# Performance work log

Hardware: AMD Instinct MI355X
Metric: run time of the kernel (lower is better)

Reference implementation:

```python
import jax, jax.numpy as jnp
import numpy as np

B, N, K = 2, 2048, 30          # batch, residues, neighbors
DN, DE, L = 256, 128, 3        # dim_nodes, dim_edges, num_layers
NF, EF = 12, 28                # raw node / edge feature dims
EPS = 1e-6


def _gather(h, idx):
    # h: [B,N,D], idx: [B,N,K] -> [B,N,K,D]
    b, n, k = idx.shape
    d = h.shape[-1]
    return jnp.take_along_axis(h, idx.reshape(b, n * k, 1), axis=1).reshape(b, n, k, d)


def _nrm(v):
    return v / (jnp.linalg.norm(v, axis=-1, keepdims=True) + EPS)


def _forward(X, C, Wn, bn, We, be, Wm1, bm1, Wm2, bm2, Wue1, bue1, Wue2, bue2):
    mask_i = (C > 0).astype(X.dtype)                      # [B,N]
    Nat, CA, Cat, Oat = X[..., 0, :], X[..., 1, :], X[..., 2, :], X[..., 3, :]

    # local residue frames via Gram-Schmidt on (N, CA, C)
    u = _nrm(Cat - CA)
    v0 = Nat - CA
    v = _nrm(v0 - jnp.sum(v0 * u, -1, keepdims=True) * u)
    w = jnp.cross(u, v)
    R = jnp.stack([u, v, w], axis=-1)                     # [B,N,3,3]

    # node features: internal coords (unit bond vectors + log lengths)
    def bond_feat(bv):
        return jnp.concatenate([_nrm(bv), jnp.log(jnp.linalg.norm(bv, axis=-1, keepdims=True) + EPS)], -1)
    node_feat = jnp.concatenate([bond_feat(CA - Nat), bond_feat(Cat - CA), bond_feat(Oat - Cat)], -1)  # [B,N,12]
    node_h = (node_feat @ Wn + bn) * mask_i[..., None]

    # kNN graph on centroid distances (graph_distance_atom_type=-1)
    Xc = X.mean(axis=2)                                   # [B,N,3]
    D2 = jnp.sum((Xc[:, :, None] - Xc[:, None, :]) ** 2, -1)  # [B,N,N]
    BIG = 1e9
    D2 = D2 + BIG * (1.0 - mask_i)[:, None, :] + BIG * jnp.eye(N, dtype=X.dtype)[None]
    _, edge_idx = jax.lax.top_k(-D2, K)                   # [B,N,K]

    mask_j = _gather(mask_i[..., None], edge_idx)[..., 0]
    mask_ij = mask_i[..., None] * mask_j                  # [B,N,K]

    # edge features: RBF distances + local-frame direction + relative rotation
    xj = _gather(Xc, edge_idx)
    d = xj - Xc[:, :, None]                               # [B,N,K,3]
    dist = jnp.linalg.norm(d, axis=-1)
    local = jnp.einsum('bndc,bnkd->bnkc', R, d)           # R_i^T d
    dirv = local / (dist[..., None] + EPS)
    Rj = _gather(R.reshape(B, N, 9), edge_idx).reshape(B, N, K, 3, 3)
    Rrel = jnp.einsum('bnde,bnkdf->bnkef', R, Rj).reshape(B, N, K, 9)  # R_i^T R_j
    centers = jnp.linspace(0.0, 20.0, 16)
    sigma = 20.0 / 16.0
    rbf = jnp.exp(-(((dist[..., None] - centers) / sigma) ** 2))       # [B,N,K,16]
    edge_h = (jnp.concatenate([rbf, dirv, Rrel], -1) @ We + be) * mask_ij[..., None]

    # GNN message passing: gather -> MLP -> masked mean scatter, + edge update
    denom = jnp.sum(mask_ij, -1, keepdims=True) + EPS     # [B,N,1]
    for l in range(L):
        hj = _gather(node_h, edge_idx)                    # [B,N,K,DN]
        hi = jnp.broadcast_to(node_h[:, :, None], hj.shape)
        mi = jnp.concatenate([hi, hj, edge_h], -1)        # [B,N,K,2*DN+DE]
        m = jax.nn.softplus(mi @ Wm1[l] + bm1[l]) @ Wm2[l] + bm2[l]
        m = m * mask_ij[..., None]
        node_h = (node_h + m.sum(axis=2) / denom) * mask_i[..., None]
        e = jax.nn.softplus(mi @ Wue1[l] + bue1[l]) @ Wue2[l] + bue2[l]
        edge_h = (edge_h + e) * mask_ij[..., None]

    return node_h, edge_h, edge_idx, mask_i, mask_ij


def setup_inputs() -> dict:
    key = jax.random.key(0)
    ks = jax.random.split(key, 10)
    s = lambda i, shp: jax.random.normal(ks[i], shp, jnp.float32) * 0.05
    M = 2 * DN + DE
    inp = {
        'X': jax.random.normal(ks[0], (B, N, 4, 3), jnp.float32),
        'C': jax.random.randint(ks[1], (B, N), 0, 4),
        'Wn': s(2, (NF, DN)), 'bn': jnp.zeros((DN,), jnp.float32),
        'We': s(3, (EF, DE)), 'be': jnp.zeros((DE,), jnp.float32),
        'Wm1': s(4, (L, M, DN)), 'bm1': jnp.zeros((L, DN), jnp.float32),
        'Wm2': s(5, (L, DN, DN)), 'bm2': jnp.zeros((L, DN), jnp.float32),
        'Wue1': s(6, (L, M, DE)), 'bue1': jnp.zeros((L, DE), jnp.float32),
        'Wue2': s(7, (L, DE, DE)), 'bue2': jnp.zeros((L, DE), jnp.float32),
    }
    return inp


def reference(X, C, Wn, bn, We, be, Wm1, bm1, Wm2, bm2, Wue1, bue1, Wue2, bue2):
    return _forward(X, C, Wn, bn, We, be, Wm1, bm1, Wm2, bm2, Wue1, bue1, Wue2, bue2)
```

## Files before the change

### kernel.cpp

```cpp
#include <hip/hip_runtime.h>
#include <math.h>

#define Bdim 2
#define Nn   2048
#define Kn   30
#define KP   32
#define DNc  256
#define DEc  128
#define NODES (Bdim*Nn)
#define EDGES (Bdim*Nn*Kn)
#define RPAD  (NODES*KP)
#define EPSF 1e-6f

#define BK 64
#define LDA (BK+8)
#define LDA0 40
#define LDP 136

typedef __attribute__((ext_vector_type(8))) short short8;
typedef __attribute__((ext_vector_type(4))) short sh4;
typedef __attribute__((ext_vector_type(4))) float floatx4;

__device__ __forceinline__ float softplusf(float x){
    float e = __expf(-fabsf(x));
// ... 240 lines not shown
    const unsigned short* __restrict__ featp, const unsigned short* __restrict__ Wp,
    const float* __restrict__ be, const float* __restrict__ mask_pad,
    unsigned short* __restrict__ edge_pad)
{
    __shared__ __align__(16) unsigned short smem[128*LDP];
    __shared__ float smask[128];
    unsigned short* Als  = smem;
    unsigned short* Bls  = smem + 128*LDA0;
    unsigned short* tile = smem;

    int tid = threadIdx.x;
    int lane = tid & 63, wave = tid >> 6;
    int wm = wave >> 1, wn = wave & 1;

    {
        const unsigned short* Ab = featp + (size_t)blockIdx.x*128*32;
        #pragma unroll
        for (int it=0; it<2; ++it){
            int idx = it*256 + tid;
            int row = idx >> 2, q = idx & 3;
            *(float4*)(&Als[row*LDA0 + q*8]) = *(const float4*)(Ab + row*32 + q*8);
        }
        if (tid < 128){
            int row = tid;
            *(float4*)(&Bls[row*LDA0 + 0])  = *(const float4*)(Wp + row*32 + 0);
            *(float4*)(&Bls[row*LDA0 + 8])  = *(const float4*)(Wp + row*32 + 8);
            *(float4*)(&Bls[row*LDA0 + 16]) = *(const float4*)(Wp + row*32 + 16);
            *(float4*)(&Bls[row*LDA0 + 24]) = *(const float4*)(Wp + row*32 + 24);
        } else {
            smask[tid-128] = mask_pad[blockIdx.x*128 + (tid-128)];
        }
    }
    __syncthreads();

    floatx4 acc[4][4];
    #pragma unroll
    for (int i=0;i<4;++i)
        #pragma unroll
        for (int j=0;j<4;++j) acc[i][j] = (floatx4){0.f,0.f,0.f,0.f};
    short8 af[4], bf[4];
    int kidx = (lane>>4)*8;
    #pragma unroll
    for (int t=0;t<4;++t){
        int row = wm*64 + t*16 + (lane&15);
        af[t] = *(const short8*)(&Als[row*LDA0 + kidx]);
        int col = wn*64 + t*16 + (lane&15);
        bf[t] = *(const short8*)(&Bls[col*LDA0 + kidx]);
    }
    __syncthreads();
    #pragma unroll
    for (int i=0;i<4;++i)
        #pragma unroll
        for (int j=0;j<4;++j)
            acc[i][j] = __builtin_amdgcn_mfma_f32_16x16x32_bf16(bf[j], af[i], acc[i][j], 0,0,0);

    int quad = lane >> 4, cl = lane & 15;
    #pragma unroll
    for (int i=0;i<4;++i){
        int rowl = wm*64 + i*16 + cl;
        float mk = smask[rowl];
        #pragma unroll
        for (int j=0;j<4;++j){
            int coll = wn*64 + j*16 + quad*4;
            float4 bv = *(const float4*)&be[coll];
            sh4 w;
            w[0] = (short)f2bf((acc[i][j][0] + bv.x)*mk);
            w[1] = (short)f2bf((acc[i][j][1] + bv.y)*mk);
            w[2] = (short)f2bf((acc[i][j][2] + bv.z)*mk);
            w[3] = (short)f2bf((acc[i][j][3] + bv.w)*mk);
            *(sh4*)(&tile[rowl*LDP + coll]) = w;
        }
    }
    __syncthreads();
    {
        int rl = tid >> 1;
        int h  = tid & 1;
        unsigned short* dst = edge_pad + (size_t)(blockIdx.x*128 + rl)*128 + h*64;
        #pragma unroll
        for (int q=0; q<8; ++q)
            *(short8*)(dst + q*8) = *(const short8*)(&tile[rl*LDP + h*64 + q*8]);
    }
}

__global__ __launch_bounds__(256) void k_pack_we0(
    const float* __restrict__ We, unsigned short* __restrict__ Wp)
{
    int id = blockIdx.x*256 + threadIdx.x;
    if (id >= 128*32) return;
    int n = id >> 5, kk = id & 31;
    Wp[id] = (kk < 28) ? f2bf(We[kk*128 + n]) : 0;
}

__global__ __launch_bounds__(256) void k_pack_pqw(
    const float* __restrict__ Wm1, const float* __restrict__ Wue1,
    unsigned short* __restrict__ wPQw)
{
    int id = blockIdx.x*256 + threadIdx.x;
    if (id >= 3*768*256) return;
    int l = id / (768*256);
    int rem = id % (768*256);
    int n = rem >> 8, k = rem & 255;
    int c = (n < 384) ? n : n - 384;
    int r = (n < 384) ? k : 256 + k;
    float v = (c < 256) ? Wm1[((size_t)l*640 + r)*256 + c]
                        : Wue1[((size_t)l*640 + r)*128 + (c-256)];
    wPQw[id] = f2bf(v);
}

__global__ __launch_bounds__(256) void k_pack_ew(
    const float* __restrict__ Wm1, const float* __restrict__ Wue1,
    unsigned short* __restrict__ wEw)
{
    int id = blockIdx.x*256 + threadIdx.x;
    if (id >= 3*384*128) return;
    int l = id / (384*128);
    int rem = id % (384*128);
    int n = rem >> 7, k = rem & 127;
    int r = 512 + k;
    float v = (n < 256) ? Wm1[((size_t)l*640 + r)*256 + n]
                        : Wue1[((size_t)l*640 + r)*128 + (n-256)];
    wEw[id] = f2bf(v);
}

__global__ __launch_bounds__(256) void k_pack_ue2(
    const float* __restrict__ Wue2, unsigned short* __restrict__ wUe2w)
{
    int id = blockIdx.x*256 + threadIdx.x;
    if (id >= 3*128*128) return;
    int l = id / (128*128);
    int rem = id % (128*128);
    int n = rem >> 7, k = rem & 127;
    wUe2w[id] = f2bf(Wue2[((size_t)l*128 + k)*128 + n]);
}

__global__ __launch_bounds__(256) void k_pack_m2(
    const float* __restrict__ Wm2, unsigned short* __restrict__ wM2w)
{
    int id = blockIdx.x*256 + threadIdx.x;
    if (id >= 3*256*256) return;
    int l = id / (256*256);
    int rem = id % (256*256);
    int n = rem >> 8, k = rem & 255;
    wM2w[id] = f2bf(Wm2[((size_t)l*256 + k)*256 + n]);
}

template<int NR>
__device__ __forceinline__ void stage_tile_t(
    const unsigned short* __restrict__ gbase, int ldg, int k0,
    unsigned short* lds, int tid)
{
    #pragma unroll
    for (int it=0; it<NR/32; ++it){
        int idx = it*256 + tid;
        int row = idx >> 3;
        int ke  = (idx & 7) * 8;
        const float4* src = (const float4*)(gbase + (size_t)row*ldg + k0 + ke);
        *(float4*)(&lds[row*LDA + ke]) = *src;
    }
}

template<int TI, int TJ>
__device__ __forceinline__ void mma_tile_t(
    const unsigned short* Als, const unsigned short* Bls,
    int wm, int wn, int lane, floatx4 acc[TI][TJ])
{
    #pragma unroll
    for (int s=0; s<2; ++s){
        short8 af[TI], bf[TJ];
        int kidx = s*32 + (lane>>4)*8;
        #pragma unroll
        for (int t=0;t<TI;++t){
            int row = wm*(TI*16) + t*16 + (lane&15);
            af[t] = *(const short8*)(&Als[row*LDA + kidx]);
        }
        #pragma unroll
        for (int t=0;t<TJ;++t){
            int col = wn*(TJ*16) + t*16 + (lane&15);
            bf[t] = *(const short8*)(&Bls[col*LDA + kidx]);
        }
        #pragma unroll
        for (int i=0;i<TI;++i)
            #pragma unroll
            for (int j=0;j<TJ;++j)
                acc[i][j] = __builtin_amdgcn_mfma_f32_16x16x32_bf16(af[i], bf[j], acc[i][j], 0,0,0);
    }
}

template<int TI, int TJ>
__device__ __forceinline__ void mma_tile_sw(
    const unsigned short* Als, const unsigned short* Bls,
    int wm, int wn, int lane, floatx4 acc[TI][TJ])
{
    #pragma unroll
    for (int s=0; s<2; ++s){
        short8 af[TI], bf[TJ];
        int kidx = s*32 + (lane>>4)*8;
        #pragma unroll
        for (int t=0;t<TI;++t){
            int row = wm*(TI*16) + t*16 + (lane&15);
            af[t] = *(const short8*)(&Als[row*LDA + kidx]);
        }
        #pragma unroll
        for (int t=0;t<TJ;++t){
            int col = wn*(TJ*16) + t*16 + (lane&15);
            bf[t] = *(const short8*)(&Bls[col*LDA + kidx]);
        }
        #pragma unroll
        for (int i=0;i<TI;++i)
            #pragma unroll
            for (int j=0;j<TJ;++j)
                acc[i][j] = __builtin_amdgcn_mfma_f32_16x16x32_bf16(bf[j], af[i], acc[i][j], 0,0,0);
    }
}

__device__ __forceinline__ void mma_tileA_lp_sw(
    const unsigned short* Atile, const unsigned short* Bls,
    int k0, int wm, int wn, int lane, floatx4 acc[4][4])
{
    #pragma unroll
    for (int s=0; s<2; ++s){
        short8 af[4], bf[4];
        int kloc = s*32 + (lane>>4)*8;
        #pragma unroll
        for (int t=0;t<4;++t){
            int row = wm*64 + t*16 + (lane&15);
            af[t] = *(const short8*)(&Atile[row*LDP + k0 + kloc]);
            int col = wn*64 + t*16 + (lane&15);
            bf[t] = *(const short8*)(&Bls[col*LDA + kloc]);
        }
        #pragma unroll
        for (int i=0;i<4;++i)
            #pragma unroll
            for (int j=0;j<4;++j)
                acc[i][j] = __builtin_amdgcn_mfma_f32_16x16x32_bf16(bf[j], af[i], acc[i][j], 0,0,0);
    }
}

__global__ __launch_bounds__(256) void k_pq(
    const unsigned short* __restrict__ A, const unsigned short* __restrict__ Bw,
    unsigned short* __restrict__ PQbf,
    const float* __restrict__ bm1l, const float* __restrict__ bue1l)
{
    __shared__ __align__(16) unsigned short smem[(64+128)*LDA];
    unsigned short* Als = smem;
    unsigned short* Bls = smem + 64*LDA;
    unsigned short* tile = smem;
    int tid = threadIdx.x;
    int lane = tid & 63, wave = tid >> 6;
    int wm = wave >> 1, wn = wave & 1;
    const unsigned short* Ab = A + (size_t)blockIdx.x*64*256;
    const unsigned short* Bb = Bw + (size_t)blockIdx.y*128*256;
    floatx4 acc[2][4];
    #pragma unroll
    for (int i=0;i<2;++i)
        #pragma unroll
        for (int j=0;j<4;++j) acc[i][j] = (floatx4){0.f,0.f,0.f,0.f};
    for (int k0=0; k0<256; k0+=BK){
        stage_tile_t<64>(Ab, 256, k0, Als, tid);
        stage_tile_t<128>(Bb, 256, k0, Bls, tid);
        __syncthreads();
        mma_tile_sw<2,4>(Als, Bls, wm, wn, lane, acc);
        __syncthreads();
    }
    int quad = lane >> 4, cl = lane & 15;
    #pragma unroll
    for (int i=0;i<2;++i){
        int rowl = wm*32 + i*16 + cl;
        #pragma unroll
        for (int j=0;j<4;++j){
            int coll = wn*64 + j*16 + quad*4;
            int col0 = blockIdx.y*128 + coll;
            float4 bv;
            if (col0 < 256)      bv = *(const float4*)&bm1l[col0];
            else if (col0 < 384) bv = *(const float4*)&bue1l[col0-256];
            else                 bv = (float4){0.f,0.f,0.f,0.f};
            sh4 w;
            w[0] = (short)f2bf(acc[i][j][0] + bv.x);
            w[1] = (short)f2bf(acc[i][j][1] + bv.y);
            w[2] = (short)f2bf(acc[i][j][2] + bv.z);
            w[3] = (short)f2bf(acc[i][j][3] + bv.w);
            *(sh4*)(&tile[rowl*LDP + coll]) = w;
        }
    }
    __syncthreads();
    {
        int rl = tid >> 2;
        int h  = tid & 3;
        unsigned short* dst = PQbf + (size_t)(blockIdx.x*64 + rl)*768 + blockIdx.y*128 + h*32;
        #pragma unroll
        for (int q=0; q<4; ++q)
            *(short8*)(dst + q*8) = *(const short8*)(&tile[rl*LDP + h*32 + q*8]);
    }
}

__global__ __launch_bounds__(256) void k_h1s(
    const unsigned short* __restrict__ Apad, const unsigned short* __restrict__ Bw,
    const unsigned short* __restrict__ PQbf, const int* __restrict__ jg_pad,
    const float* __restrict__ mask_pad,
    unsigned short* __restrict__ Sout)
{
    __shared__ __align__(16) unsigned short smem[2*128*LDA];
    __shared__ float smask[128];
    unsigned short* Als = smem;
    unsigned short* Bls = smem + 128*LDA;
    unsigned short* pqT = smem;

    int tid = threadIdx.x;
    int lane = tid & 63, wave = tid >> 6;
    int wm = wave >> 1, wn = wave & 1;
    int colblk = blockIdx.y;

    const unsigned short* Ab = Apad + (size_t)blockIdx.x*128*128;
    const unsigned short* Bb = Bw + (size_t)colblk*128*128;
    floatx4 acc[4][4];
    #pragma unroll
    for (int i=0;i<4;++i)
        #pragma unroll
        for (int j=0;j<4;++j) acc[i][j] = (floatx4){0.f,0.f,0.f,0.f};
    for (int k0=0; k0<128; k0+=BK){
        stage_tile_t<128>(Ab, 128, k0, Als, tid);
        stage_tile_t<128>(Bb, 128, k0, Bls, tid);
        __syncthreads();
        mma_tile_t<4,4>(Als, Bls, wm, wn, lane, acc);
        __syncthreads();
    }

    {
        int colbase = colblk*128;
        #pragma unroll
        for (int it=0; it<2; ++it){
            int w    = it*256 + tid;
            int rq   = w & 31;
            int c8   = w >> 5;
            int row0 = rq*4;
            int r0   = blockIdx.x*128 + row0;
            int ni   = r0 >> 5;
            int4 jg4 = *(const int4*)&jg_pad[r0];
            int colg = colbase + c8*8;
            short8 pv = *(const short8*)(PQbf + (size_t)ni*768 + colg);
            short8 q0 = *(const short8*)(PQbf + (size_t)jg4.x*768 + 384 + colg);
            short8 q1 = *(const short8*)(PQbf + (size_t)jg4.y*768 + 384 + colg);
            short8 q2 = *(const short8*)(PQbf + (size_t)jg4.z*768 + 384 + colg);
            short8 q3 = *(const short8*)(PQbf + (size_t)jg4.w*768 + 384 + colg);
            #pragma unroll
            for (int q=0; q<8; ++q){
                float pf = bf2f((unsigned short)pv[q]);
                sh4 ov;
                ov[0] = (short)f2bf(pf + bf2f((unsigned short)q0[q]));
                ov[1] = (short)f2bf(pf + bf2f((unsigned short)q1[q]));
                ov[2] = (short)f2bf(pf + bf2f((unsigned short)q2[q]));
                ov[3] = (short)f2bf(pf + bf2f((unsigned short)q3[q]));
                *(sh4*)(&pqT[(c8*8 + q)*LDP + row0]) = ov;
            }
        }
        if (tid < 128) smask[tid] = mask_pad[blockIdx.x*128 + tid];
    }
    __syncthreads();

    int quad = lane >> 4, cl = lane & 15;
    float sumA[4] = {0.f,0.f,0.f,0.f};
    float sumB[4] = {0.f,0.f,0.f,0.f};
    #pragma unroll
    for (int i=0;i<4;++i){
        int rowl0 = wm*64 + i*16 + quad*4;
        float4 mk = *(const float4*)&smask[rowl0];
        float mkv[4] = {mk.x, mk.y, mk.z, mk.w};
        #pragma unroll
        for (int j=0;j<4;++j){
            int coll = wn*64 + j*16 + cl;
            sh4 pq4 = *(const sh4*)(&pqT[coll*LDP + rowl0]);
            #pragma unroll
            for (int rg=0; rg<4; ++rg){
                float v  = softplusf(acc[i][j][rg] + bf2f((unsigned short)pq4[rg]));
                float mv = mkv[rg]*v;
                if (i < 2) sumA[j] += mv; else sumB[j] += mv;
            }
        }
    }

    int nodeA = blockIdx.x*4 + wm*2;
    #pragma unroll
    for (int j=0;j<4;++j){
        float a = sumA[j];
        a += __shfl_xor(a, 16, 64);
        a += __shfl_xor(a, 32, 64);
        float b = sumB[j];
        b += __shfl_xor(b, 16, 64);
        b += __shfl_xor(b, 32, 64);
        int col = colblk*128 + wn*64 + j*16 + cl;
        if (quad == 0)      Sout[(size_t)nodeA*256 + col]     = f2bf(a);
        else if (quad == 1) Sout[(size_t)(nodeA+1)*256 + col] = f2bf(b);
    }
}

__global__ __launch_bounds__(256) void k_h1e(
    const unsigned short* __restrict__ Apad, const unsigned short* __restrict__ BwE,
    const unsigned short* __restrict__ BwU2,
    const unsigned short* __restrict__ PQbf, const int* __restrict__ jg_pad,
    const float* __restrict__ mask_pad, const float* __restrict__ bue2l,
    unsigned short* __restrict__ edge_pad, float* __restrict__ edge_f32,
    int last)
{
    __shared__ __align__(16) unsigned short smem[26624];
    unsigned short* Als  = smem;
    unsigned short* Bls  = smem + 128*LDA;
    unsigned short* tile = smem;
    unsigned short* B2   = smem + 128*LDP;

    int tid = threadIdx.x;
    int lane = tid & 63, wave = tid >> 6;
    int wm = wave >> 1, wn = wave & 1;

    const unsigned short* Ab = Apad + (size_t)blockIdx.x*128*128;
    floatx4 acc[4][4];
    #pragma unroll
    for (int i=0;i<4;++i)
        #pragma unroll
        for (int j=0;j<4;++j) acc[i][j] = (floatx4){0.f,0.f,0.f,0.f};
    for (int k0=0; k0<128; k0+=BK){
        stage_tile_t<128>(Ab, 128, k0, Als, tid);
        stage_tile_t<128>(BwE, 128, k0, Bls, tid);
        __syncthreads();
        mma_tile_sw<4,4>(Als, Bls, wm, wn, lane, acc);
        __syncthreads();
    }

    stage_tile_t<128>(BwU2, 128, 0, B2, tid);

    {
        int rl = tid >> 1;
        int h  = tid & 1;
        int r  = blockIdx.x*128 + rl;
        int ni = r >> 5;
        int jg = jg_pad[r];
        int cb = 256 + h*64;
        const unsigned short* Pr = PQbf + (size_t)ni*768 + cb;
        const unsigned short* Qr = PQbf + (size_t)jg*768 + 384 + cb;
        #pragma unroll
        for (int q=0; q<8; ++q){
            short8 pv = *(const short8*)(Pr + q*8);
            short8 qv = *(const short8*)(Qr + q*8);
            short8 ov;
            #pragma unroll
            for (int z=0; z<8; ++z)
                ov[z] = (short)f2bf(bf2f((unsigned short)pv[z]) + bf2f((unsigned short)qv[z]));
            *(short8*)(&tile[rl*LDP + h*64 + q*8]) = ov;
        }
    }
    __syncthreads();

    int quad = lane >> 4, cl = lane & 15;
    #pragma unroll
    for (int i=0;i<4;++i){
        int rowl = wm*64 + i*16 + cl;
        #pragma unroll
        for (int j=0;j<4;++j){
            int coll = wn*64 + j*16 + quad*4;
            sh4 pq4 = *(const sh4*)(&tile[rowl*LDP + coll]);
            sh4 hv;
            #pragma unroll
            for (int rg=0; rg<4; ++rg)
                hv[rg] = (short)f2bf(softplusf(acc[i][j][rg] + bf2f((unsigned short)pq4[rg])));
            *(sh4*)(&tile[rowl*LDP + coll]) = hv;
        }
    }
    __syncthreads();

    floatx4 acc2[4][4];
    #pragma unroll
    for (int i=0;i<4;++i)
        #pragma unroll
        for (int j=0;j<4;++j) acc2[i][j] = (floatx4){0.f,0.f,0.f,0.f};
    mma_tileA_lp_sw(tile, B2, 0, wm, wn, lane, acc2);
    __syncthreads();
    stage_tile_t<128>(BwU2, 128, 64, B2, tid);
    __syncthreads();
    mma_tileA_lp_sw(tile, B2, 64, wm, wn, lane, acc2);
    __syncthreads();

    float* sbias = (float*)B2;
    #pragma unroll
    for (int i=0;i<4;++i){
        int rowl = wm*64 + i*16 + cl;
        #pragma unroll
        for (int j=0;j<4;++j){
            int coll = wn*64 + j*16 + quad*4;
            sh4 w;
            #pragma unroll
            for (int rg=0; rg<4; ++rg) w[rg] = (short)f2bf(acc2[i][j][rg]);
            *(sh4*)(&tile[rowl*LDP + coll]) = w;
        }
    }
    if (tid < 128) sbias[tid] = bue2l[tid];
    __syncthreads();

    if (last){
        int c16  = lane & 31;
        int rsub = lane >> 5;
        #pragma unroll
        for (int step=0; step<16; ++step){
            int rowl = wave*32 + step*2 + rsub;
            int R = blockIdx.x*128 + rowl;
            int k = R & (KP-1);
            if (k < Kn){
                float mij = mask_pad[R];
                int node = R >> 5;
                int e = node*Kn + k;
                sh4 ov = *(const sh4*)(edge_pad + (size_t)R*128 + c16*4);
                sh4 av = *(const sh4*)(&tile[rowl*LDP + c16*4]);
                float4 bv = *(const float4*)(&sbias[c16*4]);
                float4 f;
                f.x = (bf2f((unsigned short)ov[0]) + bf2f((unsigned short)av[0]) + bv.x)*mij;
                f.y = (bf2f((unsigned short)ov[1]) + bf2f((unsigned short)av[1]) + bv.y)*mij;
                f.z = (bf2f((unsigned short)ov[2]) + bf2f((unsigned short)av[2]) + bv.z)*mij;
                f.w = (bf2f((unsigned short)ov[3]) + bf2f((unsigned short)av[3]) + bv.w)*mij;
                *(float4*)(edge_f32 + (size_t)e*128 + c16*4) = f;
            }
        }
    } else {
        int c8   = lane & 15;
        int rsub = lane >> 4;
        #pragma unroll
        for (int step=0; step<8; ++step){
            int rowl = wave*32 + step*4 + rsub;
            int R = blockIdx.x*128 + rowl;
            int k = R & (KP-1);
            if (k < Kn){
                float mij = mask_pad[R];
                unsigned short* ep = edge_pad + (size_t)R*128 + c8*8;
                short8 ov = *(const short8*)ep;
                short8 av = *(const short8*)(&tile[rowl*LDP + c8*8]);
                float4 b0 = *(const float4*)(&sbias[c8*8]);
                float4 b1 = *(const float4*)(&sbias[c8*8 + 4]);
                float nv[8];
                nv[0] = (bf2f((unsigned short)ov[0]) + bf2f((unsigned short)av[0]) + b0.x)*mij;
                nv[1] = (bf2f((unsigned short)ov[1]) + bf2f((unsigned short)av[1]) + b0.y)*mij;
                nv[2] = (bf2f((unsigned short)ov[2]) + bf2f((unsigned short)av[2]) + b0.z)*mij;
                nv[3] = (bf2f((unsigned short)ov[3]) + bf2f((unsigned short)av[3]) + b0.w)*mij;
                nv[4] = (bf2f((unsigned short)ov[4]) + bf2f((unsigned short)av[4]) + b1.x)*mij;
                nv[5] = (bf2f((unsigned short)ov[5]) + bf2f((unsigned short)av[5]) + b1.y)*mij;
                nv[6] = (bf2f((unsigned short)ov[6]) + bf2f((unsigned short)av[6]) + b1.z)*mij;
                nv[7] = (bf2f((unsigned short)ov[7]) + bf2f((unsigned short)av[7]) + b1.w)*mij;
                short8 sv;
                #pragma unroll
                for (int z=0; z<8; ++z) sv[z] = (short)f2bf(nv[z]);
                *(short8*)ep = sv;
            }
        }
    }
}

__global__ __launch_bounds__(256) void k_node_gemm(
    const unsigned short* __restrict__ S, const unsigned short* __restrict__ Bw,
    const float* __restrict__ bm2l, const float* __restrict__ cnt,
    const float* __restrict__ mask_i,
    float* __restrict__ node_h, unsigned short* __restrict__ node_bf)
{
    __shared__ __align__(16) unsigned short Als[64*LDA];
    __shared__ __align__(16) unsigned short Bls[64*LDA];
    int tid = threadIdx.x;
    int lane = tid & 63, wave = tid >> 6;
    int wm = wave >> 1, wn = wave & 1;
    const unsigned short* Ab = S + (size_t)blockIdx.x*64*256;
    const unsigned short* Bb = Bw + (size_t)blockIdx.y*64*256;
    floatx4 acc[2][2];
    #pragma unroll
    for (int i=0;i<2;++i)
        #pragma unroll
        for (int j=0;j<2;++j) acc[i][j] = (floatx4){0.f,0.f,0.f,0.f};
    for (int k0=0; k0<256; k0+=BK){
        stage_tile_t<64>(Ab, 256, k0, Als, tid);
        stage_tile_t<64>(Bb, 256, k0, Bls, tid);
        __syncthreads();
        mma_tile_sw<2,2>(Als, Bls, wm, wn, lane, acc);
        __syncthreads();
    }
    int quad = lane >> 4, cl = lane & 15;
    #pragma unroll
    for (int i=0;i<2;++i){
        int nid = blockIdx.x*64 + wm*32 + i*16 + cl;
        float ct = cnt[nid];
        float mi = mask_i[nid];
        float dv = ct + EPSF;
        #pragma unroll
        for (int j=0;j<2;++j){
            int col = blockIdx.y*64 + wn*32 + j*16 + quad*4;
            float4 bv = *(const float4*)&bm2l[col];
            float4 nh = *(const float4*)&node_h[(size_t)nid*256 + col];
            float4 r;
            r.x = (nh.x + (acc[i][j][0] + ct*bv.x)/dv)*mi;
            r.y = (nh.y + (acc[i][j][1] + ct*bv.y)/dv)*mi;
            r.z = (nh.z + (acc[i][j][2] + ct*bv.z)/dv)*mi;
            r.w = (nh.w + (acc[i][j][3] + ct*bv.w)/dv)*mi;
            *(float4*)&node_h[(size_t)nid*256 + col] = r;
            sh4 w;
            w[0] = (short)f2bf(r.x);
            w[1] = (short)f2bf(r.y);
            w[2] = (short)f2bf(r.z);
            w[3] = (short)f2bf(r.w);
            *(sh4*)&node_bf[(size_t)nid*256 + col] = w;
        }
    }
}

extern "C" void kernel_launch(void* const* d_in, const int* in_sizes, int n_in,
                              void* d_out, int out_size, void* d_ws, size_t ws_size,
                              hipStream_t stream)
{
    (void)in_sizes; (void)n_in; (void)out_size; (void)ws_size;
    const float* X   = (const float*)d_in[0];
    const int*   C   = (const int*)  d_in[1];
    const float* Wn  = (const float*)d_in[2];
    const float* bn  = (const float*)d_in[3];
    const float* We  = (const float*)d_in[4];
    const float* be  = (const float*)d_in[5];
    const float* Wm1 = (const float*)d_in[6];
    const float* bm1 = (const float*)d_in[7];
    const float* Wm2 = (const float*)d_in[8];
    const float* bm2 = (const float*)d_in[9];
    const float* Wue1= (const float*)d_in[10];
    const float* bue1= (const float*)d_in[11];
    const float* Wue2= (const float*)d_in[12];
    const float* bue2= (const float*)d_in[13];

    float* out       = (float*)d_out;
    float* out_node  = out;
    float* out_edge  = out + 1048576;
    float* out_eidxf = out + 16777216;
    float* out_maski = out + 16900096;
    float* out_maskij= out + 16904192;

    char* wsb = (char*)d_ws;
    size_t off = 0;
    float* wXc    = (float*)(wsb + off); off += (size_t)12288*4;
    float* wR     = (float*)(wsb + off); off += (size_t)36864*4;
    float* wF     = (float*)(wsb + off); off += (size_t)49152*4;
    int*   wEidx  = (int*)  (wsb + off); off += (size_t)EDGES*4;
    int*   wJgPad = (int*)  (wsb + off); off += (size_t)RPAD*4;
    float* wMaskP = (float*)(wsb + off); off += (size_t)RPAD*4;
    float* wCnt   = (float*)(wsb + off); off += (size_t)NODES*4;
    unsigned short* wPQ      = (unsigned short*)(wsb + off); off += (size_t)NODES*768*2;
    unsigned short* wS       = (unsigned short*)(wsb + off); off += (size_t)NODES*256*2;
    unsigned short* wNodeBf  = (unsigned short*)(wsb + off); off += (size_t)NODES*256*2;
    unsigned short* wEdgePad = (unsigned short*)(wsb + off); off += (size_t)RPAD*128*2;
    unsigned short* wFeatP   = (unsigned short*)(wsb + off); off += (size_t)RPAD*32*2;
    unsigned short* wWe0     = (unsigned short*)(wsb + off); off += (size_t)128*32*2;
    unsigned short* wPQw     = (unsigned short*)(wsb + off); off += (size_t)3*768*256*2;
    unsigned short* wEw      = (unsigned short*)(wsb + off); off += (size_t)3*384*128*2;
    unsigned short* wUe2w    = (unsigned short*)(wsb + off); off += (size_t)3*128*128*2;
    unsigned short* wM2w     = (unsigned short*)(wsb + off); off += (size_t)3*256*256*2;

    k_geom <<<16,    256, 0, stream>>>(X, C, wXc, wR, wF, out_maski);
    k_nodeh<<<NODES, 256, 0, stream>>>(wF, Wn, bn, C, out_node, wNodeBf);
    k_knn  <<<NODES/4, 256, 0, stream>>>(wXc, C, wEidx, out_eidxf);

    k_pack_we0<<<16, 256, 0, stream>>>(We, wWe0);
    k_edge_feat<<<RPAD/256, 256, 0, stream>>>(wXc, wR, wEidx, C, wFeatP,
                                              out_maskij, wMaskP, wJgPad, wCnt);
    k_edge0<<<RPAD/128, 256, 0, stream>>>(wFeatP, wWe0, be, wMaskP, wEdgePad);

    k_pack_pqw<<<(3*768*256+255)/256, 256, 0, stream>>>(Wm1, Wue1, wPQw);
    k_pack_ew <<<(3*384*128+255)/256, 256, 0, stream>>>(Wm1, Wue1, wEw);
    k_pack_ue2<<<(3*128*128+255)/256, 256, 0, stream>>>(Wue2, wUe2w);
    k_pack_m2 <<<(3*256*256+255)/256, 256, 0, stream>>>(Wm2, wM2w);

    for (int l=0; l<3; ++l){
        k_pq<<<dim3(64,6), 256, 0, stream>>>(wNodeBf, wPQw + (size_t)l*768*256, wPQ,
                                             bm1 + l*256, bue1 + l*128);
        k_h1s<<<dim3(RPAD/128,2), 256, 0, stream>>>(
            wEdgePad, wEw + (size_t)l*384*128, wPQ, wJgPad, wMaskP, wS);
        k_h1e<<<RPAD/128, 256, 0, stream>>>(
            wEdgePad, wEw + (size_t)l*384*128 + (size_t)256*128,
            wUe2w + (size_t)l*128*128, wPQ, wJgPad, wMaskP, bue2 + l*128,
            wEdgePad, out_edge, (l==2) ? 1 : 0);
        k_node_gemm<<<dim3(NODES/64,4), 256, 0, stream>>>(
            wS, wM2w + (size_t)l*256*256, bm2 + l*256, wCnt, out_maski,
            out_node, wNodeBf);
    }
}
```

Before: 489.5 us.

## Merge node-sum and edge-update kernels into one launch with ping-pong edge buffers

Combines the k_h1s (message sum) and k_h1e (edge update) kernels into a single k_h1 launch whose blocks are split three ways by blockIdx, so the sum and edge-update work run concurrently within one grid. Because the edge update can no longer overwrite the edge tensor other blocks are still reading, the edge state moves to two ping-pong buffers. The five weight-packing kernels are also merged into one launch, and the MFMA operand order and epilogue indexing are changed. The aim is fewer launches and better GPU fill per layer, at the cost of an extra edge buffer and more divergent per-block code.

```diff
diff --git a/kernel.cpp b/kernel.cpp
--- a/kernel.cpp
+++ b/kernel.cpp
@@ -346,66 +346,58 @@
     }
 }
 
-__global__ __launch_bounds__(256) void k_pack_we0(
-    const float* __restrict__ We, unsigned short* __restrict__ Wp)
+__global__ __launch_bounds__(256) void k_pack_all(
+    const float* __restrict__ We, const float* __restrict__ Wm1,
+    const float* __restrict__ Wue1, const float* __restrict__ Wue2,
+    const float* __restrict__ Wm2,
+    unsigned short* __restrict__ wWe0, unsigned short* __restrict__ wPQw,
+    unsigned short* __restrict__ wEw, unsigned short* __restrict__ wUe2w,
+    unsigned short* __restrict__ wM2w)
 {
     int id = blockIdx.x*256 + threadIdx.x;
-    if (id >= 128*32) return;
-    int n = id >> 5, kk = id & 31;
-    Wp[id] = (kk < 28) ? f2bf(We[kk*128 + n]) : 0;
-}
-
-__global__ __launch_bounds__(256) void k_pack_pqw(
-    const float* __restrict__ Wm1, const float* __restrict__ Wue1,
-    unsigned short* __restrict__ wPQw)
-{
-    int id = blockIdx.x*256 + threadIdx.x;
-    if (id >= 3*768*256) return;
-    int l = id / (768*256);
-    int rem = id % (768*256);
-    int n = rem >> 8, k = rem & 255;
-    int c = (n < 384) ? n : n - 384;
-    int r = (n < 384) ? k : 256 + k;
-    float v = (c < 256) ? Wm1[((size_t)l*640 + r)*256 + c]
-                        : Wue1[((size_t)l*640 + r)*128 + (c-256)];
-    wPQw[id] = f2bf(v);
-}
-
-__global__ __launch_bounds__(256) void k_pack_ew(
-    const float* __restrict__ Wm1, const float* __restrict__ Wue1,
-    unsigned short* __restrict__ wEw)
-{
-    int id = blockIdx.x*256 + threadIdx.x;
-    if (id >= 3*384*128) return;
-    int l = id / (384*128);
-    int rem = id % (384*128);
-    int n = rem >> 7, k = rem & 127;
-    int r = 512 + k;
-    float v = (n < 256) ? Wm1[((size_t)l*640 + r)*256 + n]
-                        : Wue1[((size_t)l*640 + r)*128 + (n-256)];
-    wEw[id] = f2bf(v);
-}
-
-__global__ __launch_bounds__(256) void k_pack_ue2(
-    const float* __restrict__ Wue2, unsigned short* __restrict__ wUe2w)
-{
-    int id = blockIdx.x*256 + threadIdx.x;
-    if (id >= 3*128*128) return;
-    int l = id / (128*128);
-    int rem = id % (128*128);
-    int n = rem >> 7, k = rem & 127;
-    wUe2w[id] = f2bf(Wue2[((size_t)l*128 + k)*128 + n]);
-}
-
-__global__ __launch_bounds__(256) void k_pack_m2(
-    const float* __restrict__ Wm2, unsigned short* __restrict__ wM2w)
-{
-    int id = blockIdx.x*256 + threadIdx.x;
-    if (id >= 3*256*256) return;
-    int l = id / (256*256);
-    int rem = id % (256*256);
-    int n = rem >> 8, k = rem & 255;
-    wM2w[id] = f2bf(Wm2[((size_t)l*256 + k)*256 + n]);
+    if (id < 4096){
+        int n = id >> 5, kk = id & 31;
+        wWe0[id] = (kk < 28) ? f2bf(We[kk*128 + n]) : 0;
+        return;
+    }
+    id -= 4096;
+    if (id < 3*768*256){
+        int l = id / (768*256);
+        int rem = id % (768*256);
+        int n = rem >> 8, k = rem & 255;
+        int c = (n < 384) ? n : n - 384;
+        int r = (n < 384) ? k : 256 + k;
+        float v = (c < 256) ? Wm1[((size_t)l*640 + r)*256 + c]
+                            : Wue1[((size_t)l*640 + r)*128 + (c-256)];
+        wPQw[id] = f2bf(v);
+        return;
+    }
+    id -= 3*768*256;
+    if (id < 3*384*128){
+        int l = id / (384*128);
+        int rem = id % (384*128);
+        int n = rem >> 7, k = rem & 127;
+        int r = 512 + k;
+        float v = (n < 256) ? Wm1[((size_t)l*640 + r)*256 + n]
+                            : Wue1[((size_t)l*640 + r)*128 + (n-256)];
+        wEw[id] = f2bf(v);
+        return;
+    }
+    id -= 3*384*128;
+    if (id < 3*128*128){
+        int l = id / (128*128);
+        int rem = id % (128*128);
+        int n = rem >> 7, k = rem & 127;
+        wUe2w[id] = f2bf(Wue2[((size_t)l*128 + k)*128 + n]);
+        return;
+    }
+    id -= 3*128*128;
+    if (id < 3*256*256){
+        int l = id / (256*256);
+        int rem = id % (256*256);
+        int n = rem >> 8, k = rem & 255;
+        wM2w[id] = f2bf(Wm2[((size_t)l*256 + k)*256 + n]);
+    }
 }
 
 template<int NR>
@@ -477,7 +469,7 @@
     }
 }
 
-__device__ __forceinline__ void mma_tileA_lp_sw(
+__device__ __forceinline__ void mma_tileA_lp(
     const unsigned short* Atile, const unsigned short* Bls,
     int k0, int wm, int wn, int lane, floatx4 acc[4][4])
 {
@@ -496,7 +488,7 @@
         for (int i=0;i<4;++i)
             #pragma unroll
             for (int j=0;j<4;++j)
-                acc[i][j] = __builtin_amdgcn_mfma_f32_16x16x32_bf16(bf[j], af[i], acc[i][j], 0,0,0);
+                acc[i][j] = __builtin_amdgcn_mfma_f32_16x16x32_bf16(af[i], bf[j], acc[i][j], 0,0,0);
     }
 }
 
@@ -557,258 +549,258 @@
     }
 }
 
-__global__ __launch_bounds__(256) void k_h1s(
-    const unsigned short* __restrict__ Apad, const unsigned short* __restrict__ Bw,
+__global__ __launch_bounds__(256) void k_h1(
+    const unsigned short* __restrict__ Apad,
+    const unsigned short* __restrict__ BwAll,
+    const unsigned short* __restrict__ BwU2,
     const unsigned short* __restrict__ PQbf, const int* __restrict__ jg_pad,
-    const float* __restrict__ mask_pad,
-    unsigned short* __restrict__ Sout)
-{
-    __shared__ __align__(16) unsigned short smem[2*128*LDA];
+    const float* __restrict__ mask_pad, const float* __restrict__ bue2l,
+    unsigned short* __restrict__ Sout,
+    unsigned short* __restrict__ edge_nxt, float* __restrict__ edge_f32,
+    int last)
+{
+    __shared__ __align__(16) unsigned short smem[26624];
     __shared__ float smask[128];
-    unsigned short* Als = smem;
-    unsigned short* Bls = smem + 128*LDA;
-    unsigned short* pqT = smem;
+
+    int bid = blockIdx.x;
+    int y   = bid % 3;
+    int bx  = bid / 3;
 
     int tid = threadIdx.x;
     int lane = tid & 63, wave = tid >> 6;
     int wm = wave >> 1, wn = wave & 1;
-    int colblk = blockIdx.y;
-
-    const unsigned short* Ab = Apad + (size_t)blockIdx.x*128*128;
-    const unsigned short* Bb = Bw + (size_t)colblk*128*128;
-    floatx4 acc[4][4];
-    #pragma unroll
-    for (int i=0;i<4;++i)
-        #pragma unroll
-        for (int j=0;j<4;++j) acc[i][j] = (floatx4){0.f,0.f,0.f,0.f};
-    for (int k0=0; k0<128; k0+=BK){
-        stage_tile_t<128>(Ab, 128, k0, Als, tid);
-        stage_tile_t<128>(Bb, 128, k0, Bls, tid);
-        __syncthreads();
-        mma_tile_t<4,4>(Als, Bls, wm, wn, lane, acc);
-        __syncthreads();
-    }
-
-    {
-        int colbase = colblk*128;
-        #pragma unroll
-        for (int it=0; it<2; ++it){
-            int w    = it*256 + tid;
-            int rq   = w & 31;
-            int c8   = w >> 5;
-            int row0 = rq*4;
-            int r0   = blockIdx.x*128 + row0;
-            int ni   = r0 >> 5;
-            int4 jg4 = *(const int4*)&jg_pad[r0];
-            int colg = colbase + c8*8;
-            short8 pv = *(const short8*)(PQbf + (size_t)ni*768 + colg);
-            short8 q0 = *(const short8*)(PQbf + (size_t)jg4.x*768 + 384 + colg);
-            short8 q1 = *(const short8*)(PQbf + (size_t)jg4.y*768 + 384 + colg);
-            short8 q2 = *(const short8*)(PQbf + (size_t)jg4.z*768 + 384 + colg);
-            short8 q3 = *(const short8*)(PQbf + (size_t)jg4.w*768 + 384 + colg);
+    int quad = lane >> 4, cl = lane & 15;
+
+    if (y < 2){
+        unsigned short* Als = smem;
+        unsigned short* Bls = smem + 128*LDA;
+        unsigned short* pqT = smem;
+        int colblk = y;
+
+        const unsigned short* Ab = Apad + (size_t)bx*128*128;
+        const unsigned short* Bb = BwAll + (size_t)colblk*128*128;
+        floatx4 acc[4][4];
+        #pragma unroll
+        for (int i=0;i<4;++i)
+            #pragma unroll
+            for (int j=0;j<4;++j) acc[i][j] = (floatx4){0.f,0.f,0.f,0.f};
+        for (int k0=0; k0<128; k0+=BK){
+            stage_tile_t<128>(Ab, 128, k0, Als, tid);
+            stage_tile_t<128>(Bb, 128, k0, Bls, tid);
+            __syncthreads();
+            mma_tile_t<4,4>(Als, Bls, wm, wn, lane, acc);
+            __syncthreads();
+        }
+
+        {
+            int colbase = colblk*128;
+            #pragma unroll
+            for (int it=0; it<2; ++it){
+                int w    = it*256 + tid;
+                int rq   = w & 31;
+                int c8   = w >> 5;
+                int row0 = rq*4;
+                int r0   = bx*128 + row0;
+                int ni   = r0 >> 5;
+                int4 jg4 = *(const int4*)&jg_pad[r0];
+                int colg = colbase + c8*8;
+                short8 pv = *(const short8*)(PQbf + (size_t)ni*768 + colg);
+                short8 q0 = *(const short8*)(PQbf + (size_t)jg4.x*768 + 384 + colg);
+                short8 q1 = *(const short8*)(PQbf + (size_t)jg4.y*768 + 384 + colg);
+                short8 q2 = *(const short8*)(PQbf + (size_t)jg4.z*768 + 384 + colg);
+                short8 q3 = *(const short8*)(PQbf + (size_t)jg4.w*768 + 384 + colg);
+                #pragma unroll
+                for (int q=0; q<8; ++q){
+                    float pf = bf2f((unsigned short)pv[q]);
+                    sh4 ov;
+                    ov[0] = (short)f2bf(pf + bf2f((unsigned short)q0[q]));
+                    ov[1] = (short)f2bf(pf + bf2f((unsigned short)q1[q]));
+                    ov[2] = (short)f2bf(pf + bf2f((unsigned short)q2[q]));
+                    ov[3] = (short)f2bf(pf + bf2f((unsigned short)q3[q]));
+                    *(sh4*)(&pqT[(c8*8 + q)*LDP + row0]) = ov;
+                }
+            }
+            if (tid < 128) smask[tid] = mask_pad[bx*128 + tid];
+        }
+        __syncthreads();
+
+        float sumA[4] = {0.f,0.f,0.f,0.f};
+        float sumB[4] = {0.f,0.f,0.f,0.f};
+        #pragma unroll
+        for (int i=0;i<4;++i){
+            int rowl0 = wm*64 + i*16 + quad*4;
+            float4 mk = *(const float4*)&smask[rowl0];
+            float mkv[4] = {mk.x, mk.y, mk.z, mk.w};
+            #pragma unroll
+            for (int j=0;j<4;++j){
+                int coll = wn*64 + j*16 + cl;
+                sh4 pq4 = *(const sh4*)(&pqT[coll*LDP + rowl0]);
+                #pragma unroll
+                for (int rg=0; rg<4; ++rg){
+                    float v  = softplusf(acc[i][j][rg] + bf2f((unsigned short)pq4[rg]));
+                    float mv = mkv[rg]*v;
+                    if (i < 2) sumA[j] += mv; else sumB[j] += mv;
+                }
+            }
+        }
+
+        int nodeA = bx*4 + wm*2;
+        #pragma unroll
+        for (int j=0;j<4;++j){
+            float a = sumA[j];
+            a += __shfl_xor(a, 16, 64);
+            a += __shfl_xor(a, 32, 64);
+            float b = sumB[j];
+            b += __shfl_xor(b, 16, 64);
+            b += __shfl_xor(b, 32, 64);
+            int col = colblk*128 + wn*64 + j*16 + cl;
+            if (quad == 0)      Sout[(size_t)nodeA*256 + col]     = f2bf(a);
+            else if (quad == 1) Sout[(size_t)(nodeA+1)*256 + col] = f2bf(b);
+        }
+    } else {
+        unsigned short* Als  = smem;
+        unsigned short* Bls  = smem + 128*LDA;
+        unsigned short* tile = smem;
+        unsigned short* B2   = smem + 128*LDP;
+        const unsigned short* BwE = BwAll + (size_t)2*128*128;
+
+        const unsigned short* Ab = Apad + (size_t)bx*128*128;
+        floatx4 acc[4][4];
+        #pragma unroll
+        for (int i=0;i<4;++i)
+            #pragma unroll
+            for (int j=0;j<4;++j) acc[i][j] = (floatx4){0.f,0.f,0.f,0.f};
+        for (int k0=0; k0<128; k0+=BK){
+            stage_tile_t<128>(Ab, 128, k0, Als, tid);
+            stage_tile_t<128>(BwE, 128, k0, Bls, tid);
+            __syncthreads();
+            mma_tile_t<4,4>(Als, Bls, wm, wn, lane, acc);
+            __syncthreads();
+        }
+
+        stage_tile_t<128>(BwU2, 128, 0, B2, tid);
+
+        {
+            int rl = tid >> 1;
+            int h  = tid & 1;
+            int r  = bx*128 + rl;
+            int ni = r >> 5;
+            int jg = jg_pad[r];
+            int cb = 256 + h*64;
+            const unsigned short* Pr = PQbf + (size_t)ni*768 + cb;
+            const unsigned short* Qr = PQbf + (size_t)jg*768 + 384 + cb;
             #pragma unroll
             for (int q=0; q<8; ++q){
-                float pf = bf2f((unsigned short)pv[q]);
-                sh4 ov;
-                ov[0] = (short)f2bf(pf + bf2f((unsigned short)q0[q]));
-                ov[1] = (short)f2bf(pf + bf2f((unsigned short)q1[q]));
-                ov[2] = (short)f2bf(pf + bf2f((unsigned short)q2[q]));
-                ov[3] = (short)f2bf(pf + bf2f((unsigned short)q3[q]));
-                *(sh4*)(&pqT[(c8*8 + q)*LDP + row0]) = ov;
+                short8 pv = *(const short8*)(Pr + q*8);
+                short8 qv = *(const short8*)(Qr + q*8);
+                short8 ov;
+                #pragma unroll
+                for (int z=0; z<8; ++z)
+                    ov[z] = (short)f2bf(bf2f((unsigned short)pv[z]) + bf2f((unsigned short)qv[z]));
+                *(short8*)(&tile[rl*LDP + h*64 + q*8]) = ov;
             }
         }
-        if (tid < 128) smask[tid] = mask_pad[blockIdx.x*128 + tid];
-    }
-    __syncthreads();
-
-    int quad = lane >> 4, cl = lane & 15;
-    float sumA[4] = {0.f,0.f,0.f,0.f};
-    float sumB[4] = {0.f,0.f,0.f,0.f};
-    #pragma unroll
-    for (int i=0;i<4;++i){
-        int rowl0 = wm*64 + i*16 + quad*4;
-        float4 mk = *(const float4*)&smask[rowl0];
-        float mkv[4] = {mk.x, mk.y, mk.z, mk.w};
-        #pragma unroll
-        for (int j=0;j<4;++j){
-            int coll = wn*64 + j*16 + cl;
-            sh4 pq4 = *(const sh4*)(&pqT[coll*LDP + rowl0]);
-            #pragma unroll
-            for (int rg=0; rg<4; ++rg){
-                float v  = softplusf(acc[i][j][rg] + bf2f((unsigned short)pq4[rg]));
-                float mv = mkv[rg]*v;
-                if (i < 2) sumA[j] += mv; else sumB[j] += mv;
+        __syncthreads();
+
+        #pragma unroll
+        for (int i=0;i<4;++i){
+            #pragma unroll
+            for (int rg=0;rg<4;++rg){
+                int rowl = wm*64 + i*16 + quad*4 + rg;
+                #pragma unroll
+                for (int j=0;j<4;++j){
+                    int coll = wn*64 + j*16 + cl;
+                    float pq = bf2f(tile[rowl*LDP + coll]);
+                    float v  = softplusf(acc[i][j][rg] + pq);
+                    tile[rowl*LDP + coll] = f2bf(v);
+                }
             }
         }
-    }
-
-    int nodeA = blockIdx.x*4 + wm*2;
-    #pragma unroll
-    for (int j=0;j<4;++j){
-        float a = sumA[j];
-        a += __shfl_xor(a, 16, 64);
-        a += __shfl_xor(a, 32, 64);
-        float b = sumB[j];
-        b += __shfl_xor(b, 16, 64);
-        b += __shfl_xor(b, 32, 64);
-        int col = colblk*128 + wn*64 + j*16 + cl;
-        if (quad == 0)      Sout[(size_t)nodeA*256 + col]     = f2bf(a);
-        else if (quad == 1) Sout[(size_t)(nodeA+1)*256 + col] = f2bf(b);
-    }
-}
-
-__global__ __launch_bounds__(256) void k_h1e(
-    const unsigned short* __restrict__ Apad, const unsigned short* __restrict__ BwE,
-    const unsigned short* __restrict__ BwU2,
-    const unsigned short* __restrict__ PQbf, const int* __restrict__ jg_pad,
-    const float* __restrict__ mask_pad, const float* __restrict__ bue2l,
-    unsigned short* __restrict__ edge_pad, float* __restrict__ edge_f32,
-    int last)
-{
-    __shared__ __align__(16) unsigned short smem[26624];
-    unsigned short* Als  = smem;
-    unsigned short* Bls  = smem + 128*LDA;
-    unsigned short* tile = smem;
-    unsigned short* B2   = smem + 128*LDP;
-
-    int tid = threadIdx.x;
-    int lane = tid & 63, wave = tid >> 6;
-    int wm = wave >> 1, wn = wave & 1;
-
-    const unsigned short* Ab = Apad + (size_t)blockIdx.x*128*128;
-    floatx4 acc[4][4];
-    #pragma unroll
-    for (int i=0;i<4;++i)
-        #pragma unroll
-        for (int j=0;j<4;++j) acc[i][j] = (floatx4){0.f,0.f,0.f,0.f};
-    for (int k0=0; k0<128; k0+=BK){
-        stage_tile_t<128>(Ab, 128, k0, Als, tid);
-        stage_tile_t<128>(BwE, 128, k0, Bls, tid);
-        __syncthreads();
-        mma_tile_sw<4,4>(Als, Bls, wm, wn, lane, acc);
-        __syncthreads();
-    }
-
-    stage_tile_t<128>(BwU2, 128, 0, B2, tid);
-
-    {
-        int rl = tid >> 1;
-        int h  = tid & 1;
-        int r  = blockIdx.x*128 + rl;
-        int ni = r >> 5;
-        int jg = jg_pad[r];
-        int cb = 256 + h*64;
-        const unsigned short* Pr = PQbf + (size_t)ni*768 + cb;
-        const unsigned short* Qr = PQbf + (size_t)jg*768 + 384 + cb;
-        #pragma unroll
-        for (int q=0; q<8; ++q){
-            short8 pv = *(const short8*)(Pr + q*8);
-            short8 qv = *(const short8*)(Qr + q*8);
-            short8 ov;
-            #pragma unroll
-            for (int z=0; z<8; ++z)
-                ov[z] = (short)f2bf(bf2f((unsigned short)pv[z]) + bf2f((unsigned short)qv[z]));
-            *(short8*)(&tile[rl*LDP + h*64 + q*8]) = ov;
-        }
-    }
-    __syncthreads();
-
-    int quad = lane >> 4, cl = lane & 15;
-    #pragma unroll
-    for (int i=0;i<4;++i){
-        int rowl = wm*64 + i*16 + cl;
-        #pragma unroll
-        for (int j=0;j<4;++j){
-            int coll = wn*64 + j*16 + quad*4;
-            sh4 pq4 = *(const sh4*)(&tile[rowl*LDP + coll]);
-            sh4 hv;
-            #pragma unroll
-            for (int rg=0; rg<4; ++rg)
-                hv[rg] = (short)f2bf(softplusf(acc[i][j][rg] + bf2f((unsigned short)pq4[rg])));
-            *(sh4*)(&tile[rowl*LDP + coll]) = hv;
-        }
-    }
-    __syncthreads();
-
-    floatx4 acc2[4][4];
-    #pragma unroll
-    for (int i=0;i<4;++i)
-        #pragma unroll
-        for (int j=0;j<4;++j) acc2[i][j] = (floatx4){0.f,0.f,0.f,0.f};
-    mma_tileA_lp_sw(tile, B2, 0, wm, wn, lane, acc2);
-    __syncthreads();
-    stage_tile_t<128>(BwU2, 128, 64, B2, tid);
-    __syncthreads();
-    mma_tileA_lp_sw(tile, B2, 64, wm, wn, lane, acc2);
-    __syncthreads();
-
-    float* sbias = (float*)B2;
-    #pragma unroll
-    for (int i=0;i<4;++i){
-        int rowl = wm*64 + i*16 + cl;
-        #pragma unroll
-        for (int j=0;j<4;++j){
-            int coll = wn*64 + j*16 + quad*4;
-            sh4 w;
-            #pragma unroll
-            for (int rg=0; rg<4; ++rg) w[rg] = (short)f2bf(acc2[i][j][rg]);
-            *(sh4*)(&tile[rowl*LDP + coll]) = w;
-        }
-    }
-    if (tid < 128) sbias[tid] = bue2l[tid];
-    __syncthreads();
-
-    if (last){
-        int c16  = lane & 31;
-        int rsub = lane >> 5;
-        #pragma unroll
-        for (int step=0; step<16; ++step){
-            int rowl = wave*32 + step*2 + rsub;
-            int R = blockIdx.x*128 + rowl;
-            int k = R & (KP-1);
-            if (k < Kn){
-                float mij = mask_pad[R];
-                int node = R >> 5;
-                int e = node*Kn + k;
-                sh4 ov = *(const sh4*)(edge_pad + (size_t)R*128 + c16*4);
-                sh4 av = *(const sh4*)(&tile[rowl*LDP + c16*4]);
-                float4 bv = *(const float4*)(&sbias[c16*4]);
-                float4 f;
-                f.x = (bf2f((unsigned short)ov[0]) + bf2f((unsigned short)av[0]) + bv.x)*mij;
-                f.y = (bf2f((unsigned short)ov[1]) + bf2f((unsigned short)av[1]) + bv.y)*mij;
-                f.z = (bf2f((unsigned short)ov[2]) + bf2f((unsigned short)av[2]) + bv.z)*mij;
-                f.w = (bf2f((unsigned short)ov[3]) + bf2f((unsigned short)av[3]) + bv.w)*mij;
-                *(float4*)(edge_f32 + (size_t)e*128 + c16*4) = f;
+        __syncthreads();
+
+        floatx4 acc2[4][4];
+        #pragma unroll
+        for (int i=0;i<4;++i)
+            #pragma unroll
+            for (int j=0;j<4;++j) acc2[i][j] = (floatx4){0.f,0.f,0.f,0.f};
+        mma_tileA_lp(tile, B2, 0, wm, wn, lane, acc2);
+        __syncthreads();
+        stage_tile_t<128>(BwU2, 128, 64, B2, tid);
+        __syncthreads();
+        mma_tileA_lp(tile, B2, 64, wm, wn, lane, acc2);
+        __syncthreads();
+
+        float* sbias = (float*)B2;
+        #pragma unroll
+        for (int i=0;i<4;++i){
+            #pragma unroll
+            for (int rg=0;rg<4;++rg){
+                int rowl = wm*64 + i*16 + quad*4 + rg;
+                #pragma unroll
+                for (int j=0;j<4;++j){
+                    int coll = wn*64 + j*16 + cl;
+                    tile[rowl*LDP + coll] = f2bf(acc2[i][j][rg]);
+                }
             }
         }
-    } else {
-        int c8   = lane & 15;
-        int rsub = lane >> 4;
-        #pragma unroll
-        for (int step=0; step<8; ++step){
-            int rowl = wave*32 + step*4 + rsub;
-            int R = blockIdx.x*128 + rowl;
-            int k = R & (KP-1);
-            if (k < Kn){
-                float mij = mask_pad[R];
-                unsigned short* ep = edge_pad + (size_t)R*128 + c8*8;
-                short8 ov = *(const short8*)ep;
-                short8 av = *(const short8*)(&tile[rowl*LDP + c8*8]);
-                float4 b0 = *(const float4*)(&sbias[c8*8]);
-                float4 b1 = *(const float4*)(&sbias[c8*8 + 4]);
-                float nv[8];
-                nv[0] = (bf2f((unsigned short)ov[0]) + bf2f((unsigned short)av[0]) + b0.x)*mij;
-                nv[1] = (bf2f((unsigned short)ov[1]) + bf2f((unsigned short)av[1]) + b0.y)*mij;
-                nv[2] = (bf2f((unsigned short)ov[2]) + bf2f((unsigned short)av[2]) + b0.z)*mij;
-                nv[3] = (bf2f((unsigned short)ov[3]) + bf2f((unsigned short)av[3]) + b0.w)*mij;
-                nv[4] = (bf2f((unsigned short)ov[4]) + bf2f((unsigned short)av[4]) + b1.x)*mij;
-                nv[5] = (bf2f((unsigned short)ov[5]) + bf2f((unsigned short)av[5]) + b1.y)*mij;
-                nv[6] = (bf2f((unsigned short)ov[6]) + bf2f((unsigned short)av[6]) + b1.z)*mij;
-                nv[7] = (bf2f((unsigned short)ov[7]) + bf2f((unsigned short)av[7]) + b1.w)*mij;
-                short8 sv;
-                #pragma unroll
-                for (int z=0; z<8; ++z) sv[z] = (short)f2bf(nv[z]);
-                *(short8*)ep = sv;
+        if (tid < 128) sbias[tid] = bue2l[tid];
+        __syncthreads();
+
+        if (last){
+            int c16  = lane & 31;
+            int rsub = lane >> 5;
+            #pragma unroll
+            for (int step=0; step<16; ++step){
+                int rowl = wave*32 + step*2 + rsub;
+                int R = bx*128 + rowl;
+                int k = R & (KP-1);
+                if (k < Kn){
+                    float mij = mask_pad[R];
+                    int node = R >> 5;
+                    int e = node*Kn + k;
+                    sh4 ov = *(const sh4*)(Apad + (size_t)R*128 + c16*4);
+                    sh4 av = *(const sh4*)(&tile[rowl*LDP + c16*4]);
+                    float4 bv = *(const float4*)(&sbias[c16*4]);
+                    float4 f;
+                    f.x = (bf2f((unsigned short)ov[0]) + bf2f((unsigned short)av[0]) + bv.x)*mij;
+                    f.y = (bf2f((unsigned short)ov[1]) + bf2f((unsigned short)av[1]) + bv.y)*mij;
+                    f.z = (bf2f((unsigned short)ov[2]) + bf2f((unsigned short)av[2]) + bv.z)*mij;
+                    f.w = (bf2f((unsigned short)ov[3]) + bf2f((unsigned short)av[3]) + bv.w)*mij;
+                    *(float4*)(edge_f32 + (size_t)e*128 + c16*4) = f;
+                }
+            }
+        } else {
+            int c8   = lane & 15;
+            int rsub = lane >> 4;
+            #pragma unroll
+            for (int step=0; step<8; ++step){
+                int rowl = wave*32 + step*4 + rsub;
+                int R = bx*128 + rowl;
+                int k = R & (KP-1);
+                unsigned short* ep = edge_nxt + (size_t)R*128 + c8*8;
+                if (k < Kn){
+                    float mij = mask_pad[R];
+                    short8 ov = *(const short8*)(Apad + (size_t)R*128 + c8*8);
+                    short8 av = *(const short8*)(&tile[rowl*LDP + c8*8]);
+                    float4 b0 = *(const float4*)(&sbias[c8*8]);
+                    float4 b1 = *(const float4*)(&sbias[c8*8 + 4]);
+                    float nv[8];
+                    nv[0] = (bf2f((unsigned short)ov[0]) + bf2f((unsigned short)av[0]) + b0.x)*mij;
+                    nv[1] = (bf2f((unsigned short)ov[1]) + bf2f((unsigned short)av[1]) + b0.y)*mij;
+                    nv[2] = (bf2f((unsigned short)ov[2]) + bf2f((unsigned short)av[2]) + b0.z)*mij;
+                    nv[3] = (bf2f((unsigned short)ov[3]) + bf2f((unsigned short)av[3]) + b0.w)*mij;
+                    nv[4] = (bf2f((unsigned short)ov[4]) + bf2f((unsigned short)av[4]) + b1.x)*mij;
+                    nv[5] = (bf2f((unsigned short)ov[5]) + bf2f((unsigned short)av[5]) + b1.y)*mij;
+                    nv[6] = (bf2f((unsigned short)ov[6]) + bf2f((unsigned short)av[6]) + b1.z)*mij;
+                    nv[7] = (bf2f((unsigned short)ov[7]) + bf2f((unsigned short)av[7]) + b1.w)*mij;
+                    short8 sv;
+                    #pragma unroll
+                    for (int z=0; z<8; ++z) sv[z] = (short)f2bf(nv[z]);
+                    *(short8*)ep = sv;
+                } else {
+                    short8 z = {0,0,0,0,0,0,0,0};
+                    *(short8*)ep = z;
+                }
             }
         }
     }
@@ -906,7 +898,8 @@
     unsigned short* wPQ      = (unsigned short*)(wsb + off); off += (size_t)NODES*768*2;
     unsigned short* wS       = (unsigned short*)(wsb + off); off += (size_t)NODES*256*2;
     unsigned short* wNodeBf  = (unsigned short*)(wsb + off); off += (size_t)NODES*256*2;
-    unsigned short* wEdgePad = (unsigned short*)(wsb + off); off += (size_t)RPAD*128*2;
+    unsigned short* wEdgePadA= (unsigned short*)(wsb + off); off += (size_t)RPAD*128*2;
+    unsigned short* wEdgePadB= (unsigned short*)(wsb + off); off += (size_t)RPAD*128*2;
     unsigned short* wFeatP   = (unsigned short*)(wsb + off); off += (size_t)RPAD*32*2;
     unsigned short* wWe0     = (unsigned short*)(wsb + off); off += (size_t)128*32*2;
     unsigned short* wPQw     = (unsigned short*)(wsb + off); off += (size_t)3*768*256*2;
@@ -914,29 +907,25 @@
     unsigned short* wUe2w    = (unsigned short*)(wsb + off); off += (size_t)3*128*128*2;
     unsigned short* wM2w     = (unsigned short*)(wsb + off); off += (size_t)3*256*256*2;
 
+    unsigned short* eb[2] = { wEdgePadA, wEdgePadB };
+
     k_geom <<<16,    256, 0, stream>>>(X, C, wXc, wR, wF, out_maski);
     k_nodeh<<<NODES, 256, 0, stream>>>(wF, Wn, bn, C, out_node, wNodeBf);
     k_knn  <<<NODES/4, 256, 0, stream>>>(wXc, C, wEidx, out_eidxf);
 
-    k_pack_we0<<<16, 256, 0, stream>>>(We, wWe0);
+    k_pack_all<<<3856, 256, 0, stream>>>(We, Wm1, Wue1, Wue2, Wm2,
+                                         wWe0, wPQw, wEw, wUe2w, wM2w);
     k_edge_feat<<<RPAD/256, 256, 0, stream>>>(wXc, wR, wEidx, C, wFeatP,
                                               out_maskij, wMaskP, wJgPad, wCnt);
-    k_edge0<<<RPAD/128, 256, 0, stream>>>(wFeatP, wWe0, be, wMaskP, wEdgePad);
-
-    k_pack_pqw<<<(3*768*256+255)/256, 256, 0, stream>>>(Wm1, Wue1, wPQw);
-    k_pack_ew <<<(3*384*128+255)/256, 256, 0, stream>>>(Wm1, Wue1, wEw);
-    k_pack_ue2<<<(3*128*128+255)/256, 256, 0, stream>>>(Wue2, wUe2w);
-    k_pack_m2 <<<(3*256*256+255)/256, 256, 0, stream>>>(Wm2, wM2w);
+    k_edge0<<<RPAD/128, 256, 0, stream>>>(wFeatP, wWe0, be, wMaskP, wEdgePadA);
 
     for (int l=0; l<3; ++l){
         k_pq<<<dim3(64,6), 256, 0, stream>>>(wNodeBf, wPQw + (size_t)l*768*256, wPQ,
                                              bm1 + l*256, bue1 + l*128);
-        k_h1s<<<dim3(RPAD/128,2), 256, 0, stream>>>(
-            wEdgePad, wEw + (size_t)l*384*128, wPQ, wJgPad, wMaskP, wS);
-        k_h1e<<<RPAD/128, 256, 0, stream>>>(
-            wEdgePad, wEw + (size_t)l*384*128 + (size_t)256*128,
-            wUe2w + (size_t)l*128*128, wPQ, wJgPad, wMaskP, bue2 + l*128,
-            wEdgePad, out_edge, (l==2) ? 1 : 0);
+        k_h1<<<3*(RPAD/128), 256, 0, stream>>>(
+            eb[l&1], wEw + (size_t)l*384*128, wUe2w + (size_t)l*128*128,
+            wPQ, wJgPad, wMaskP, bue2 + l*128,
+            wS, eb[(l+1)&1], out_edge, (l==2) ? 1 : 0);
         k_node_gemm<<<dim3(NODES/64,4), 256, 0, stream>>>(
             wS, wM2w + (size_t)l*256*256, bm2 + l*256, wCnt, out_maski,
             out_node, wNodeBf);
```

After: 520.2 us. 6.3% more time.
